# Kernel tuning notes

Hardware: AMD Instinct MI355X
Metric: run time of the kernel (lower is better)

The kernel has to match this reference:

```python
import jax, jax.numpy as jnp
import numpy as np
from jax import lax

# 5x5 Gaussian kernel, sigma=1.0 (matches cv2.getGaussianKernel(5, 1.0))
_xs = np.arange(5) - 2
_k1 = np.exp(-(_xs ** 2) / 2.0)
_k1 = (_k1 / _k1.sum()).astype(np.float32)
_K2 = jnp.asarray(np.outer(_k1, _k1))  # [5,5]


def _blur(x):
    """Gaussian blur on [B,H,W] with BORDER_REFLECT_101 (cv2 default)."""
    xp = jnp.pad(x, ((0, 0), (2, 2), (2, 2)), mode='reflect')
    y = lax.conv_general_dilated(xp[:, None], _K2[None, None], (1, 1), 'VALID')
    return y[:, 0]


def _hist_entropy(noise):
    """Per-image 50-bin histogram entropy over range (-0.5, 0.5). noise: [B,H,W]."""
    def one(v):
        h, _ = jnp.histogram(v, bins=50, range=(-0.5, 0.5))
        h = h.astype(jnp.float32)
        p = h / (h.sum() + 1e-10)
        return -jnp.sum(p * jnp.log2(p + 1e-10))
    return jax.vmap(one)(noise.reshape(noise.shape[0], -1))


def _noise_features(x):
    # x: [B,3,H,W] float in [0,1]
    # gray path: quantize to uint8 (truncation), cv2 RGB2GRAY weights w/ rounding
    xq = jnp.floor(jnp.clip(x * 255.0, 0.0, 255.0))  # uint8 truncation
    gray = jnp.round(0.299 * xq[:, 0] + 0.587 * xq[:, 1] + 0.114 * xq[:, 2]) / 255.0
    noise = gray - _blur(gray)  # [B,H,W]
    local_var = jnp.var(noise, axis=(1, 2))
    noise_std = jnp.std(noise, axis=(1, 2))
    entropy = _hist_entropy(noise)
    # per-channel noise std on the float image (no quantization in original)
    B, C, H, W = x.shape
    ch = x.reshape(B * C, H, W)
    ch_noise = ch - _blur(ch)
    ch_std = jnp.std(ch_noise, axis=(1, 2)).reshape(B, C)
    return jnp.stack([local_var, noise_std, entropy], axis=1).astype(jnp.float32)\
        , ch_std


def setup_inputs() -> dict:
    key = jax.random.key(0)
    ks = jax.random.split(key, 5)
    B, H, W = 64, 512, 512
    x = jax.random.uniform(ks[0], (B, 3, H, W), dtype=jnp.float32)
    # torch Linear weights: [out, in], kaiming-uniform-ish init
    W1 = jax.random.uniform(ks[1], (32, 6), minval=-1, maxval=1) / np.sqrt(6)
    b1 = jax.random.uniform(ks[2], (32,), minval=-1, maxval=1) / np.sqrt(6)
    W2 = jax.random.uniform(ks[3], (64, 32), minval=-1, maxval=1) / np.sqrt(32)
    b2 = jax.random.uniform(ks[4], (64,), minval=-1, maxval=1) / np.sqrt(32)
    return {"x": x, "W1": W1, "b1": b1, "W2": W2, "b2": b2}


def reference(x, W1, b1, W2, b2):
    stats, ch_std = _noise_features(x)
    feats = jnp.concatenate([stats, ch_std], axis=1)  # [B,6]
    h = jax.nn.relu(feats @ W1.T + b1)  # dropout in eval mode = identity
    return jax.nn.relu(h @ W2.T + b2)
```

## Files before the change

### kernel.cpp

```cpp
#include <hip/hip_runtime.h>
#include <math.h>

#define HH 512
#define WW 512
#define NB 64
#define CH_STRIDE (HH*WW)
#define IMG_STRIDE (3*CH_STRIDE)

#define GK0 0.0544886846f
#define GK1 0.2442013419f
#define GK2 0.4026199468f

__device__ __forceinline__ float quant255(float v) {
    return floorf(fminf(fmaxf(__fmul_rn(v, 255.0f), 0.0f), 255.0f));
}
__device__ __forceinline__ float gray255(float qa, float qb, float qc) {
    return rintf(__fadd_rn(__fadd_rn(__fmul_rn(0.299f, qa), __fmul_rn(0.587f, qb)),
                           __fmul_rn(0.114f, qc)));
}

__global__ __launch_bounds__(256)
void noise_main(const float* __restrict__ x, float* __restrict__ gsums,
                unsigned int* __restrict__ ghist)
{
    __shared__ unsigned int lhist[4][50];
    const int tid  = threadIdx.x;
    const int lane = tid & 63;
    const int wid  = tid >> 6;
    if (tid < 200) ((unsigned int*)lhist)[tid] = 0u;
    __syncthreads();

    const int blk   = blockIdx.x;
    const int b     = blk >> 4;
    const int strip = (blk >> 3) & 1;
    const int cg    = blk & 7;
    const int chunk = cg * 4 + wid;
    const int R0    = chunk * 16;
    const int X0    = strip * 256;
    const int gcol  = X0 + lane * 4;

    const float* pa = x + (size_t)b * IMG_STRIDE;
    const float* pb = pa + CH_STRIDE;
    const float* pc = pb + CH_STRIDE;

    float hrA[5][4], hrB[5][4], hrC[5][4], hrG[5][4];
    float d1A[4], d1B[4], d1C[4], d1G[4];
    float d2A[4], d2B[4], d2C[4], d2G[4];
    float sA=0.f,qA=0.f,sB=0.f,qB=0.f,sC=0.f,qC=0.f,sG=0.f,qG=0.f;

    #pragma unroll 1
    for (int tb = 0; tb < 4; ++tb) {
        #pragma unroll
        for (int u = 0; u < 5; ++u) {
            const int t = tb * 5 + u;
            int r = R0 - 2 + t;
            r = (r < 0) ? -r : ((r >= HH) ? (2*(HH-1) - r) : r);
            const int rowoff = r * WW;
            const float4 va = *(const float4*)(pa + rowoff + gcol);
            const float4 vb = *(const float4*)(pb + rowoff + gcol);
            const float4 vc = *(const float4*)(pc + rowoff + gcol);

            float l2a = __shfl_up(va.z, 1), l1a = __shfl_up(va.w, 1);
            float l2b = __shfl_up(vb.z, 1), l1b = __shfl_up(vb.w, 1);
            float l2c = __shfl_up(vc.z, 1), l1c = __shfl_up(vc.w, 1);
            float r0a = __shfl_down(va.x, 1), r1a = __shfl_down(va.y, 1);
            float r0b = __shfl_down(vb.x, 1), r1b = __shfl_down(vb.y, 1);
            float r0c = __shfl_down(vc.x, 1), r1c = __shfl_down(vc.y, 1);
            if (lane == 0) {
                if (X0 == 0) {
                    l2a = va.z; l1a = va.y; l2b = vb.z; l1b = vb.y; l2c = vc.z; l1c = vc.y;
                } else {
                    float2 e;
                    e = *(const float2*)(pa + rowoff + 254); l2a = e.x; l1a = e.y;
                    e = *(const float2*)(pb + rowoff + 254); l2b = e.x; l1b = e.y;
                    e = *(const float2*)(pc + rowoff + 254); l2c = e.x; l1c = e.y;
                }
            }
            if (lane == 63) {
                if (X0 == 0) {
                    float2 e;
                    e = *(const float2*)(pa + rowoff + 256); r0a = e.x; r1a = e.y;
                    e = *(const float2*)(pb + rowoff + 256); r0b = e.x; r1b = e.y;
                    e = *(const float2*)(pc + rowoff + 256); r0c = e.x; r1c = e.y;
                } else {
                    r0a = va.z; r1a = va.y; r0b = vb.z; r1b = vb.y; r0c = vc.z; r1c = vc.y;
                }
            }

            float g0 = gray255(quant255(va.x), quant255(vb.x), quant255(vc.x));
            float g1 = gray255(quant255(va.y), quant255(vb.y), quant255(vc.y));
            float g2 = gray255(quant255(va.z), quant255(vb.z), quant255(vc.z));
            float g3 = gray255(quant255(va.w), quant255(vb.w), quant255(vc.w));
            float gl2 = gray255(quant255(l2a), quant255(l2b), quant255(l2c));
            float gl1 = gray255(quant255(l1a), quant255(l1b), quant255(l1c));
            float gr0 = gray255(quant255(r0a), quant255(r0b), quant255(r0c));
            float gr1 = gray255(quant255(r1a), quant255(r1b), quant255(r1c));

            hrA[u][0] = GK0*(l2a+va.z) + GK1*(l1a+va.y) + GK2*va.x;
            hrA[u][1] = GK0*(l1a+va.w) + GK1*(va.x+va.z) + GK2*va.y;
            hrA[u][2] = GK0*(va.x+r0a) + GK1*(va.y+va.w) + GK2*va.z;
            hrA[u][3] = GK0*(va.y+r1a) + GK1*(va.z+r0a) + GK2*va.w;
            hrB[u][0] = GK0*(l2b+vb.z) + GK1*(l1b+vb.y) + GK2*vb.x;
            hrB[u][1] = GK0*(l1b+vb.w) + GK1*(vb.x+vb.z) + GK2*vb.y;
            hrB[u][2] = GK0*(vb.x+r0b) + GK1*(vb.y+vb.w) + GK2*vb.z;
            hrB[u][3] = GK0*(vb.y+r1b) + GK1*(vb.z+r0b) + GK2*vb.w;
            hrC[u][0] = GK0*(l2c+vc.z) + GK1*(l1c+vc.y) + GK2*vc.x;
            hrC[u][1] = GK0*(l1c+vc.w) + GK1*(vc.x+vc.z) + GK2*vc.y;
            hrC[u][2] = GK0*(vc.x+r0c) + GK1*(vc.y+vc.w) + GK2*vc.z;
            hrC[u][3] = GK0*(vc.y+r1c) + GK1*(vc.z+r0c) + GK2*vc.w;
            hrG[u][0] = GK0*(gl2+g2) + GK1*(gl1+g1) + GK2*g0;
            hrG[u][1] = GK0*(gl1+g3) + GK1*(g0+g2)  + GK2*g1;
            hrG[u][2] = GK0*(g0+gr0) + GK1*(g1+g3)  + GK2*g2;
            hrG[u][3] = GK0*(g1+gr1) + GK1*(g2+gr0) + GK2*g3;

            if (t >= 4) {
                const int s0=(u+1)%5, s1=(u+2)%5, s2=(u+3)%5, s3=(u+4)%5, s4=u;
                #pragma unroll
                for (int j = 0; j < 4; ++j) {
                    float bl, v;
                    bl = GK0*(hrA[s0][j]+hrA[s4][j]) + GK1*(hrA[s1][j]+hrA[s3][j]) + GK2*hrA[s2][j];
                    v  = d2A[j] - bl;  sA += v;  qA = fmaf(v, v, qA);
                    bl = GK0*(hrB[s0][j]+hrB[s4][j]) + GK1*(hrB[s1][j]+hrB[s3][j]) + GK2*hrB[s2][j];
                    v  = d2B[j] - bl;  sB += v;  qB = fmaf(v, v, qB);
                    bl = GK0*(hrC[s0][j]+hrC[s4][j]) + GK1*(hrC[s1][j]+hrC[s3][j]) + GK2*hrC[s2][j];
                    v  = d2C[j] - bl;  sC += v;  qC = fmaf(v, v, qC);
                    bl = GK0*(hrG[s0][j]+hrG[s4][j]) + GK1*(hrG[s1][j]+hrG[s3][j]) + GK2*hrG[s2][j];
                    v  = d2G[j] - bl;  sG += v;  qG = fmaf(v, v, qG);
                    if (v >= -127.5f && v <= 127.5f) {
                        int idx = (int)((v + 127.5f) * 0.19607843137254902f);
                        idx = idx > 49 ? 49 : idx;
                        atomicAdd(&lhist[wid][idx], 1u);
                    }
                }
            }

            #pragma unroll
            for (int j = 0; j < 4; ++j) { d2A[j]=d1A[j]; d2B[j]=d1B[j]; d2C[j]=d1C[j]; d2G[j]=d1G[j]; }
            d1A[0]=va.x; d1A[1]=va.y; d1A[2]=va.z; d1A[3]=va.w;
            d1B[0]=vb.x; d1B[1]=vb.y; d1B[2]=vb.z; d1B[3]=vb.w;
            d1C[0]=vc.x; d1C[1]=vc.y; d1C[2]=vc.z; d1C[3]=vc.w;
            d1G[0]=g0;   d1G[1]=g1;   d1G[2]=g2;   d1G[3]=g3;
        }
    }

    float acc[8] = {sA, qA, sB, qB, sC, qC, sG, qG};
    #pragma unroll
    for (int f = 0; f < 8; ++f) {
        float v = acc[f];
        #pragma unroll
        for (int o = 32; o > 0; o >>= 1) v += __shfl_down(v, o);
        if (lane == 0) atomicAdd(&gsums[b*8 + f], v);
    }
    __syncthreads();
    if (tid < 50) {
        unsigned int h = lhist[0][tid] + lhist[1][tid] + lhist[2][tid] + lhist[3][tid];
        atomicAdd(&ghist[b*50 + tid], h);
    }
}

__global__ __launch_bounds__(64)
void noise_final(const float* __restrict__ gsums, const unsigned int* __restrict__ ghist,
                 const float* __restrict__ W1, const float* __restrict__ b1,
                 const float* __restrict__ W2, const float* __restrict__ b2,
                 float* __restrict__ out)
{
    const int b = blockIdx.x;
    const int k = threadIdx.x;
    const float invN = 1.0f / (float)(HH*WW);
    float feats[6];
    {
        float s = gsums[b*8 + 6], q = gsums[b*8 + 7];
        float m = s * invN;
        float var255 = q * invN - m*m;
        var255 = var255 < 0.f ? 0.f : var255;
        float var = var255 * (1.0f/65025.0f);
        feats[0] = var; feats[1] = sqrtf(var);
    }
    {
        float tot = 0.f;
        for (int i = 0; i < 50; ++i) tot += (float)ghist[b*50 + i];
        float inv = 1.0f / (tot + 1e-10f);
        float e = 0.f;
        for (int i = 0; i < 50; ++i) {
            float p = (float)ghist[b*50 + i] * inv;
            e -= p * log2f(p + 1e-10f);
        }
        feats[2] = e;
    }
    for (int c = 0; c < 3; ++c) {
        float s = gsums[b*8 + 2*c], q = gsums[b*8 + 2*c + 1];
        float m = s * invN;
        float v = q * invN - m*m;
        feats[3+c] = sqrtf(v < 0.f ? 0.f : v);
    }
    float h[32];
    #pragma unroll
    for (int i = 0; i < 32; ++i) {
        float a = b1[i];
        #pragma unroll
        for (int j = 0; j < 6; ++j) a = fmaf(feats[j], W1[i*6 + j], a);
        h[i] = a > 0.f ? a : 0.f;
    }
    float a = b2[k];
    #pragma unroll
    for (int j = 0; j < 32; ++j) a = fmaf(h[j], W2[k*32 + j], a);
    out[b*64 + k] = a > 0.f ? a : 0.f;
}

extern "C" void kernel_launch(void* const* d_in, const int* in_sizes, int n_in,
                              void* d_out, int out_size, void* d_ws, size_t ws_size,
                              hipStream_t stream) {
    (void)in_sizes; (void)n_in; (void)out_size; (void)ws_size;
    const float* x  = (const float*)d_in[0];
    const float* W1 = (const float*)d_in[1];
    const float* b1 = (const float*)d_in[2];
    const float* W2 = (const float*)d_in[3];
    const float* b2 = (const float*)d_in[4];
    float* out = (float*)d_out;

    float* gsums = (float*)d_ws;
    unsigned int* ghist = (unsigned int*)((char*)d_ws + NB*8*4);
    hipMemsetAsync(d_ws, 0, NB*8*4 + NB*50*4, stream);

    hipLaunchKernelGGL(noise_main, dim3(1024), dim3(256), 0, stream, x, gsums, ghist);
    hipLaunchKernelGGL(noise_final, dim3(64), dim3(64), 0, stream,
                       gsums, ghist, W1, b1, W2, b2, out);
}
```

Measured before the change: 355.1 us.

## Split fused noise kernel into per-channel and gray histogram kernels

```diff
diff --git a/kernel.cpp b/kernel.cpp
--- a/kernel.cpp
+++ b/kernel.cpp
@@ -11,6 +11,9 @@
 #define GK1 0.2442013419f
 #define GK2 0.4026199468f
 
+#define WS_GRAY_OFF 384
+#define WS_FLOATS   512
+
 __device__ __forceinline__ float quant255(float v) {
     return floorf(fminf(fmaxf(__fmul_rn(v, 255.0f), 0.0f), 255.0f));
 }
@@ -18,16 +21,90 @@
     return rintf(__fadd_rn(__fadd_rn(__fmul_rn(0.299f, qa), __fmul_rn(0.587f, qb)),
                            __fmul_rn(0.114f, qc)));
 }
+__device__ __forceinline__ int reflect_row(int r) {
+    return (r < 0) ? -r : ((r >= HH) ? (2*(HH-1) - r) : r);
+}
+
 
 __global__ __launch_bounds__(256)
-void noise_main(const float* __restrict__ x, float* __restrict__ gsums,
-                unsigned int* __restrict__ ghist)
+void ch_noise(const float* __restrict__ x, float* __restrict__ gsums)
 {
-    __shared__ unsigned int lhist[4][50];
     const int tid  = threadIdx.x;
     const int lane = tid & 63;
     const int wid  = tid >> 6;
-    if (tid < 200) ((unsigned int*)lhist)[tid] = 0u;
+
+    const int blk   = blockIdx.x;
+    const int plane = blk >> 4;
+    const int strip = (blk >> 3) & 1;
+    const int cg    = blk & 7;
+    const int chunk = cg * 4 + wid;
+    const int R0    = chunk * 16;
+    const int X0    = strip * 256;
+    const int gcol  = X0 + lane * 4;
+
+    const float* p = x + (size_t)plane * CH_STRIDE;
+
+    float hr[5][4];
+    float d1[4], d2[4];
+    float s = 0.f, q = 0.f;
+
+    #pragma unroll 1
+    for (int tb = 0; tb < 4; ++tb) {
+        #pragma unroll
+        for (int u = 0; u < 5; ++u) {
+            const int t = tb * 5 + u;
+            const int rowoff = reflect_row(R0 - 2 + t) * WW;
+            const float4 v4 = *(const float4*)(p + rowoff + gcol);
+
+            float l2 = __shfl_up(v4.z, 1), l1 = __shfl_up(v4.w, 1);
+            float r0 = __shfl_down(v4.x, 1), r1 = __shfl_down(v4.y, 1);
+            if (lane == 0) {
+                if (X0 == 0) { l2 = v4.z; l1 = v4.y; }
+                else { float2 e = *(const float2*)(p + rowoff + 254); l2 = e.x; l1 = e.y; }
+            }
+            if (lane == 63) {
+                if (X0 == 0) { float2 e = *(const float2*)(p + rowoff + 256); r0 = e.x; r1 = e.y; }
+                else { r0 = v4.z; r1 = v4.y; }
+            }
+
+            hr[u][0] = GK0*(l2+v4.z)  + GK1*(l1+v4.y)   + GK2*v4.x;
+            hr[u][1] = GK0*(l1+v4.w)  + GK1*(v4.x+v4.z) + GK2*v4.y;
+            hr[u][2] = GK0*(v4.x+r0)  + GK1*(v4.y+v4.w) + GK2*v4.z;
+            hr[u][3] = GK0*(v4.y+r1)  + GK1*(v4.z+r0)   + GK2*v4.w;
+
+            if (t >= 4) {
+                const int s0=(u+1)%5, s1=(u+2)%5, s2=(u+3)%5, s3=(u+4)%5, s4=u;
+                #pragma unroll
+                for (int j = 0; j < 4; ++j) {
+                    float bl = GK0*(hr[s0][j]+hr[s4][j]) + GK1*(hr[s1][j]+hr[s3][j]) + GK2*hr[s2][j];
+                    float v  = d2[j] - bl;
+                    s += v;  q = fmaf(v, v, q);
+                }
+            }
+            #pragma unroll
+            for (int j = 0; j < 4; ++j) d2[j] = d1[j];
+            d1[0]=v4.x; d1[1]=v4.y; d1[2]=v4.z; d1[3]=v4.w;
+        }
+    }
+
+    #pragma unroll
+    for (int o = 32; o > 0; o >>= 1) { s += __shfl_down(s, o); q += __shfl_down(q, o); }
+    if (lane == 0) {
+        atomicAdd(&gsums[plane*2 + 0], s);
+        atomicAdd(&gsums[plane*2 + 1], q);
+    }
+}
+
+__global__ __launch_bounds__(256)
+void gray_hist(const float* __restrict__ x, float* __restrict__ gsums,
+               unsigned int* __restrict__ ghist)
+{
+    __shared__ unsigned int lhist[16][50];
+    const int tid  = threadIdx.x;
+    const int lane = tid & 63;
+    const int wid  = tid >> 6;
+    const int rep  = tid >> 4;
+    for (int i = tid; i < 16*50; i += 256) ((unsigned int*)lhist)[i] = 0u;
     __syncthreads();
 
     const int blk   = blockIdx.x;
@@ -43,117 +120,83 @@
     const float* pb = pa + CH_STRIDE;
     const float* pc = pb + CH_STRIDE;
 
-    float hrA[5][4], hrB[5][4], hrC[5][4], hrG[5][4];
-    float d1A[4], d1B[4], d1C[4], d1G[4];
-    float d2A[4], d2B[4], d2C[4], d2G[4];
-    float sA=0.f,qA=0.f,sB=0.f,qB=0.f,sC=0.f,qC=0.f,sG=0.f,qG=0.f;
+    float hr[5][4];
+    float d1[4], d2[4];
+    float s = 0.f, q = 0.f;
 
     #pragma unroll 1
     for (int tb = 0; tb < 4; ++tb) {
         #pragma unroll
         for (int u = 0; u < 5; ++u) {
             const int t = tb * 5 + u;
-            int r = R0 - 2 + t;
-            r = (r < 0) ? -r : ((r >= HH) ? (2*(HH-1) - r) : r);
-            const int rowoff = r * WW;
+            const int rowoff = reflect_row(R0 - 2 + t) * WW;
             const float4 va = *(const float4*)(pa + rowoff + gcol);
             const float4 vb = *(const float4*)(pb + rowoff + gcol);
             const float4 vc = *(const float4*)(pc + rowoff + gcol);
-
-            float l2a = __shfl_up(va.z, 1), l1a = __shfl_up(va.w, 1);
-            float l2b = __shfl_up(vb.z, 1), l1b = __shfl_up(vb.w, 1);
-            float l2c = __shfl_up(vc.z, 1), l1c = __shfl_up(vc.w, 1);
-            float r0a = __shfl_down(va.x, 1), r1a = __shfl_down(va.y, 1);
-            float r0b = __shfl_down(vb.x, 1), r1b = __shfl_down(vb.y, 1);
-            float r0c = __shfl_down(vc.x, 1), r1c = __shfl_down(vc.y, 1);
-            if (lane == 0) {
-                if (X0 == 0) {
-                    l2a = va.z; l1a = va.y; l2b = vb.z; l1b = vb.y; l2c = vc.z; l1c = vc.y;
-                } else {
-                    float2 e;
-                    e = *(const float2*)(pa + rowoff + 254); l2a = e.x; l1a = e.y;
-                    e = *(const float2*)(pb + rowoff + 254); l2b = e.x; l1b = e.y;
-                    e = *(const float2*)(pc + rowoff + 254); l2c = e.x; l1c = e.y;
-                }
-            }
-            if (lane == 63) {
-                if (X0 == 0) {
-                    float2 e;
-                    e = *(const float2*)(pa + rowoff + 256); r0a = e.x; r1a = e.y;
-                    e = *(const float2*)(pb + rowoff + 256); r0b = e.x; r1b = e.y;
-                    e = *(const float2*)(pc + rowoff + 256); r0c = e.x; r1c = e.y;
-                } else {
-                    r0a = va.z; r1a = va.y; r0b = vb.z; r1b = vb.y; r0c = vc.z; r1c = vc.y;
-                }
-            }
 
             float g0 = gray255(quant255(va.x), quant255(vb.x), quant255(vc.x));
             float g1 = gray255(quant255(va.y), quant255(vb.y), quant255(vc.y));
             float g2 = gray255(quant255(va.z), quant255(vb.z), quant255(vc.z));
             float g3 = gray255(quant255(va.w), quant255(vb.w), quant255(vc.w));
-            float gl2 = gray255(quant255(l2a), quant255(l2b), quant255(l2c));
-            float gl1 = gray255(quant255(l1a), quant255(l1b), quant255(l1c));
-            float gr0 = gray255(quant255(r0a), quant255(r0b), quant255(r0c));
-            float gr1 = gray255(quant255(r1a), quant255(r1b), quant255(r1c));
-
-            hrA[u][0] = GK0*(l2a+va.z) + GK1*(l1a+va.y) + GK2*va.x;
-            hrA[u][1] = GK0*(l1a+va.w) + GK1*(va.x+va.z) + GK2*va.y;
-            hrA[u][2] = GK0*(va.x+r0a) + GK1*(va.y+va.w) + GK2*va.z;
-            hrA[u][3] = GK0*(va.y+r1a) + GK1*(va.z+r0a) + GK2*va.w;
-            hrB[u][0] = GK0*(l2b+vb.z) + GK1*(l1b+vb.y) + GK2*vb.x;
-            hrB[u][1] = GK0*(l1b+vb.w) + GK1*(vb.x+vb.z) + GK2*vb.y;
-            hrB[u][2] = GK0*(vb.x+r0b) + GK1*(vb.y+vb.w) + GK2*vb.z;
-            hrB[u][3] = GK0*(vb.y+r1b) + GK1*(vb.z+r0b) + GK2*vb.w;
-            hrC[u][0] = GK0*(l2c+vc.z) + GK1*(l1c+vc.y) + GK2*vc.x;
-            hrC[u][1] = GK0*(l1c+vc.w) + GK1*(vc.x+vc.z) + GK2*vc.y;
-            hrC[u][2] = GK0*(vc.x+r0c) + GK1*(vc.y+vc.w) + GK2*vc.z;
-            hrC[u][3] = GK0*(vc.y+r1c) + GK1*(vc.z+r0c) + GK2*vc.w;
-            hrG[u][0] = GK0*(gl2+g2) + GK1*(gl1+g1) + GK2*g0;
-            hrG[u][1] = GK0*(gl1+g3) + GK1*(g0+g2)  + GK2*g1;
-            hrG[u][2] = GK0*(g0+gr0) + GK1*(g1+g3)  + GK2*g2;
-            hrG[u][3] = GK0*(g1+gr1) + GK1*(g2+gr0) + GK2*g3;
+
+            float gl2 = __shfl_up(g2, 1),  gl1 = __shfl_up(g3, 1);
+            float gr0 = __shfl_down(g0, 1), gr1 = __shfl_down(g1, 1);
+            if (lane == 0) {
+                if (X0 == 0) { gl2 = g2; gl1 = g1; }
+                else {
+                    float2 ea = *(const float2*)(pa + rowoff + 254);
+                    float2 eb = *(const float2*)(pb + rowoff + 254);
+                    float2 ec = *(const float2*)(pc + rowoff + 254);
+                    gl2 = gray255(quant255(ea.x), quant255(eb.x), quant255(ec.x));
+                    gl1 = gray255(quant255(ea.y), quant255(eb.y), quant255(ec.y));
+                }
+            }
+            if (lane == 63) {
+                if (X0 == 0) {
+                    float2 ea = *(const float2*)(pa + rowoff + 256);
+                    float2 eb = *(const float2*)(pb + rowoff + 256);
+                    float2 ec = *(const float2*)(pc + rowoff + 256);
+                    gr0 = gray255(quant255(ea.x), quant255(eb.x), quant255(ec.x));
+                    gr1 = gray255(quant255(ea.y), quant255(eb.y), quant255(ec.y));
+                } else { gr0 = g2; gr1 = g1; }
+            }
+
+            hr[u][0] = GK0*(gl2+g2) + GK1*(gl1+g1) + GK2*g0;
+            hr[u][1] = GK0*(gl1+g3) + GK1*(g0+g2)  + GK2*g1;
+            hr[u][2] = GK0*(g0+gr0) + GK1*(g1+g3)  + GK2*g2;
+            hr[u][3] = GK0*(g1+gr1) + GK1*(g2+gr0) + GK2*g3;
 
             if (t >= 4) {
                 const int s0=(u+1)%5, s1=(u+2)%5, s2=(u+3)%5, s3=(u+4)%5, s4=u;
                 #pragma unroll
                 for (int j = 0; j < 4; ++j) {
-                    float bl, v;
-                    bl = GK0*(hrA[s0][j]+hrA[s4][j]) + GK1*(hrA[s1][j]+hrA[s3][j]) + GK2*hrA[s2][j];
-                    v  = d2A[j] - bl;  sA += v;  qA = fmaf(v, v, qA);
-                    bl = GK0*(hrB[s0][j]+hrB[s4][j]) + GK1*(hrB[s1][j]+hrB[s3][j]) + GK2*hrB[s2][j];
-                    v  = d2B[j] - bl;  sB += v;  qB = fmaf(v, v, qB);
-                    bl = GK0*(hrC[s0][j]+hrC[s4][j]) + GK1*(hrC[s1][j]+hrC[s3][j]) + GK2*hrC[s2][j];
-                    v  = d2C[j] - bl;  sC += v;  qC = fmaf(v, v, qC);
-                    bl = GK0*(hrG[s0][j]+hrG[s4][j]) + GK1*(hrG[s1][j]+hrG[s3][j]) + GK2*hrG[s2][j];
-                    v  = d2G[j] - bl;  sG += v;  qG = fmaf(v, v, qG);
+                    float bl = GK0*(hr[s0][j]+hr[s4][j]) + GK1*(hr[s1][j]+hr[s3][j]) + GK2*hr[s2][j];
+                    float v  = d2[j] - bl;
+                    s += v;  q = fmaf(v, v, q);
                     if (v >= -127.5f && v <= 127.5f) {
                         int idx = (int)((v + 127.5f) * 0.19607843137254902f);
                         idx = idx > 49 ? 49 : idx;
-                        atomicAdd(&lhist[wid][idx], 1u);
+                        atomicAdd(&lhist[rep][idx], 1u);
                     }
                 }
             }
-
             #pragma unroll
-            for (int j = 0; j < 4; ++j) { d2A[j]=d1A[j]; d2B[j]=d1B[j]; d2C[j]=d1C[j]; d2G[j]=d1G[j]; }
-            d1A[0]=va.x; d1A[1]=va.y; d1A[2]=va.z; d1A[3]=va.w;
-            d1B[0]=vb.x; d1B[1]=vb.y; d1B[2]=vb.z; d1B[3]=vb.w;
-            d1C[0]=vc.x; d1C[1]=vc.y; d1C[2]=vc.z; d1C[3]=vc.w;
-            d1G[0]=g0;   d1G[1]=g1;   d1G[2]=g2;   d1G[3]=g3;
+            for (int j = 0; j < 4; ++j) d2[j] = d1[j];
+            d1[0]=g0; d1[1]=g1; d1[2]=g2; d1[3]=g3;
         }
     }
 
-    float acc[8] = {sA, qA, sB, qB, sC, qC, sG, qG};
-    #pragma unroll
-    for (int f = 0; f < 8; ++f) {
-        float v = acc[f];
-        #pragma unroll
-        for (int o = 32; o > 0; o >>= 1) v += __shfl_down(v, o);
-        if (lane == 0) atomicAdd(&gsums[b*8 + f], v);
+    #pragma unroll
+    for (int o = 32; o > 0; o >>= 1) { s += __shfl_down(s, o); q += __shfl_down(q, o); }
+    if (lane == 0) {
+        atomicAdd(&gsums[WS_GRAY_OFF + b*2 + 0], s);
+        atomicAdd(&gsums[WS_GRAY_OFF + b*2 + 1], q);
     }
     __syncthreads();
     if (tid < 50) {
-        unsigned int h = lhist[0][tid] + lhist[1][tid] + lhist[2][tid] + lhist[3][tid];
+        unsigned int h = 0;
+        #pragma unroll
+        for (int rr = 0; rr < 16; ++rr) h += lhist[rr][tid];
         atomicAdd(&ghist[b*50 + tid], h);
     }
 }
@@ -169,7 +212,7 @@
     const float invN = 1.0f / (float)(HH*WW);
     float feats[6];
     {
-        float s = gsums[b*8 + 6], q = gsums[b*8 + 7];
+        float s = gsums[WS_GRAY_OFF + b*2 + 0], q = gsums[WS_GRAY_OFF + b*2 + 1];
         float m = s * invN;
         float var255 = q * invN - m*m;
         var255 = var255 < 0.f ? 0.f : var255;
@@ -188,7 +231,7 @@
         feats[2] = e;
     }
     for (int c = 0; c < 3; ++c) {
-        float s = gsums[b*8 + 2*c], q = gsums[b*8 + 2*c + 1];
+        float s = gsums[(b*3 + c)*2 + 0], q = gsums[(b*3 + c)*2 + 1];
         float m = s * invN;
         float v = q * invN - m*m;
         feats[3+c] = sqrtf(v < 0.f ? 0.f : v);
@@ -219,10 +262,11 @@
     float* out = (float*)d_out;
 
     float* gsums = (float*)d_ws;
-    unsigned int* ghist = (unsigned int*)((char*)d_ws + NB*8*4);
-    hipMemsetAsync(d_ws, 0, NB*8*4 + NB*50*4, stream);
-
-    hipLaunchKernelGGL(noise_main, dim3(1024), dim3(256), 0, stream, x, gsums, ghist);
+    unsigned int* ghist = (unsigned int*)((char*)d_ws + WS_FLOATS*4);
+    hipMemsetAsync(d_ws, 0, WS_FLOATS*4 + NB*50*4, stream);
+
+    hipLaunchKernelGGL(ch_noise,  dim3(3072), dim3(256), 0, stream, x, gsums);
+    hipLaunchKernelGGL(gray_hist, dim3(1024), dim3(256), 0, stream, x, gsums, ghist);
     hipLaunchKernelGGL(noise_final, dim3(64), dim3(64), 0, stream,
                        gsums, ghist, W1, b1, W2, b2, out);
 }
```

Result: slower. 391.1 us (+10.1%).
